# Optimization experiments

Measured on AMD Instinct MI355X. Metric: run time of the kernel, lower is better.

Reference implementation:

```python
import jax, jax.numpy as jnp
import numpy as np

N_LEVELS, CPL = 4, 1024           # levels, cells per level (n_cells = 4096)
IN_D, HID, OUT_D, MLP = 512, 1024, 512, 128


def setup_inputs() -> dict:
    key = jax.random.key(0)
    ks = iter(jax.random.split(key, 32))
    r = lambda shape, s=0.05: jax.random.normal(next(ks), shape, dtype=jnp.float32) * s
    inp = {
        'x': r((1, IN_D), 1.0),
        'hiddens': r((N_LEVELS * CPL, HID), 0.1),
        'ea_W1': r((N_LEVELS, IN_D + HID, MLP)), 'ea_b1': r((N_LEVELS, MLP)),
        'ea_W2': r((N_LEVELS, MLP, OUT_D)),      'ea_b2': r((N_LEVELS, OUT_D)),
        'eg_W1': r((N_LEVELS, IN_D + HID, MLP)), 'eg_b1': r((N_LEVELS, MLP)),
        'eg_W2': r((N_LEVELS, MLP, OUT_D)),      'eg_b2': r((N_LEVELS, OUT_D)),
        'gru_Wih': r((N_LEVELS, 3 * HID, OUT_D + 1)),
        'gru_Whh': r((N_LEVELS, 3 * HID, HID)),
        'gru_bih': r((N_LEVELS, 3 * HID)), 'gru_bhh': r((N_LEVELS, 3 * HID)),
        'pred_W1': r((N_LEVELS - 1, HID, HID)), 'pred_b1': r((N_LEVELS - 1, HID)),
        'pred_W2': r((N_LEVELS - 1, HID, HID)), 'pred_b2': r((N_LEVELS - 1, HID)),
        'pei_W': r((HID * N_LEVELS, OUT_D)), 'pei_b': r((OUT_D,)),
        'step': 10,
    }
    return inp


def _forward(x, hiddens, ea_W1, ea_b1, ea_W2, ea_b2, eg_W1, eg_b1, eg_W2, eg_b2,
             gru_Wih, gru_Whh, gru_bih, gru_bhh, pred_W1, pred_b1, pred_W2, pred_b2,
             pei_W, pei_b, step):
    L = gru_Whh.shape[0]
    Hd = gru_Whh.shape[2]
    C = hiddens.shape[0] // L
    h = hiddens.reshape(L, C, Hd)                              # [L,C,H]
    xb = jnp.broadcast_to(x[0], (L, C, x.shape[-1]))           # same x for every cell
    comb = jnp.concatenate([xb, h], axis=-1)                   # [L,C,IN+H]

    def mlp(W1, b1, W2, b2):
        z = jax.nn.relu(jnp.einsum('lci,lim->lcm', comb, W1) + b1[:, None, :])
        return jnp.einsum('lcm,lmo->lco', z, W2) + b2[:, None, :]

    out = mlp(ea_W1, ea_b1, ea_W2, ea_b2) - mlp(eg_W1, eg_b1, eg_W2, eg_b2)  # a - g
    tension = jnp.mean(out ** 2, axis=-1, keepdims=True)       # [L,C,1]
    avg_tension = jnp.mean(tension)                            # mean over all cells

    # GRUCell (torch gate order r,z,n); mem input is detached in the original
    mem_in = jax.lax.stop_gradient(jnp.concatenate([out, tension], axis=-1))  # [L,C,OUT+1]
    gi = jnp.einsum('lci,lgi->lcg', mem_in, gru_Wih) + gru_bih[:, None, :]
    gh = jnp.einsum('lch,lgh->lcg', h, gru_Whh) + gru_bhh[:, None, :]
    i_r, i_z, i_n = jnp.split(gi, 3, axis=-1)
    h_r, h_z, h_n = jnp.split(gh, 3, axis=-1)
    rg = jax.nn.sigmoid(i_r + h_r)
    zg = jax.nn.sigmoid(i_z + h_z)
    ng = jnp.tanh(i_n + rg * h_n)
    new_h = jax.lax.stop_gradient((1.0 - zg) * ng + zg * h)    # self.hiddens = ...detach()

    level_means = new_h.mean(axis=1)                           # [L,H] (pre pe-update)

    # top-down predictors: predicted[lv] from level_means[lv+1]
    pz = jax.nn.relu(jnp.einsum('li,lim->lm', level_means[1:], pred_W1) + pred_b1)
    predicted = jnp.einsum('lm,lmo->lo', pz, pred_W2) + pred_b2          # [L-1,H]
    pe_signal = jax.lax.stop_gradient((predicted - level_means[:-1]) * 0.05)
    delta = jnp.zeros_like(level_means).at[:-1].add(pe_signal).at[1:].add(-0.5 * pe_signal)
    hh = new_h + delta[:, None, :]

    # per-level mean blend
    hh = 0.85 * hh + 0.15 * hh.mean(axis=1, keepdims=True)
    # faction sync: with n_factions == n_levels, factions == levels exactly
    hh = 0.85 * hh + 0.15 * hh.mean(axis=1, keepdims=True)
    if step > 5:  # debate (step is a static Python int)
        global_op = hh.mean(axis=1).mean(axis=0)               # [H]
        dc = max(1, C // 4)
        hh = hh.at[:, :dc].set(0.85 * hh[:, :dc] + 0.15 * global_op)

    combined = level_means.reshape(-1) @ pei_W + pei_b         # [OUT]
    return combined, avg_tension, hh.reshape(-1, Hd)


def reference(x, hiddens, ea_W1, ea_b1, ea_W2, ea_b2, eg_W1, eg_b1, eg_W2, eg_b2,
              gru_Wih, gru_Whh, gru_bih, gru_bhh, pred_W1, pred_b1, pred_W2, pred_b2,
              pei_W, pei_b, step):
    return _forward(x, hiddens, ea_W1, ea_b1, ea_W2, ea_b2, eg_W1, eg_b1, eg_W2, eg_b2,
                    gru_Wih, gru_Whh, gru_bih, gru_bhh, pred_W1, pred_b1, pred_W2, pred_b2,
                    pei_W, pei_b, step)
```

## Files before the change

### kernel.cpp

```cpp
#include <hip/hip_runtime.h>
#include <math.h>

#define L4   4
#define CPL  1024
#define HID  1024
#define IND  512
#define MLPD 128
#define OUTD 512
#define G3   3072
#define ROWS 4096
#define KP   544

typedef unsigned short u16;
typedef u16   u16x8  __attribute__((ext_vector_type(8)));
typedef short bf16x8 __attribute__((ext_vector_type(8)));
typedef float f32x4  __attribute__((ext_vector_type(4)));

__device__ __forceinline__ float b2f(u16 u) {
  return __uint_as_float(((unsigned int)u) << 16);
}
__device__ __forceinline__ u16 f2b(float f) {
  unsigned int x = __float_as_uint(f);
  x += 0x7fffu + ((x >> 16) & 1u);
  return (u16)(x >> 16);
}
__device__ __forceinline__ float sigm(float v) { return 1.0f/(1.0f + expf(-v)); }

struct F4 { float x, y, z, w; };
__device__ __forceinline__ float ld1(const void* p, size_t i, bool f32) {
  return f32 ? ((const float*)p)[i] : b2f(((const u16*)p)[i]);
}
__device__ __forceinline__ void st1(void* p, size_t i, float v, bool f32) {
  if (f32) ((float*)p)[i] = v; else ((u16*)p)[i] = f2b(v);
}
__device__ __forceinline__ u16x8 ldc8(const void* p, size_t i, bool f32) {
  u16x8 r;
  if (f32) {
    const float* q = (const float*)p + i;
    float4 v0 = *reinterpret_cast<const float4*>(q);
    float4 v1 = *reinterpret_cast<const float4*>(q + 4);
    r[0]=f2b(v0.x); r[1]=f2b(v0.y); r[2]=f2b(v0.z); r[3]=f2b(v0.w);
    r[4]=f2b(v1.x); r[5]=f2b(v1.y); r[6]=f2b(v1.z); r[7]=f2b(v1.w);
  } else {
    r = *reinterpret_cast<const u16x8*>((const u16*)p + i);
  }
  return r;
}

__global__ void k_detect(const void* __restrict__ x, int* __restrict__ flag) {
  int t = threadIdx.x;
  const u16* xu = (const u16*)x;
  unsigned u = xu[2*t];
  int e = (u >> 7) & 0xFF;
  int good = (e >= 96 && e <= 134) ? 1 : 0;
  __shared__ int cnt[256];
  cnt[t] = good;
  __syncthreads();
  for (int s = 128; s > 0; s >>= 1) { if (t < s) cnt[t] += cnt[t+s]; __syncthreads(); }
  if (t == 0) flag[0] = (cnt[0] < 200) ? 1 : 0;
}

__global__ void k_prep(float* __restrict__ zf, const void* __restrict__ bih,
                       const void* __restrict__ bhh, const int* __restrict__ dflag,
                       float* __restrict__ bs_r, float* __restrict__ bs_z,
                       float* __restrict__ bn_i, float* __restrict__ bn_h) {
  const bool f32 = dflag[0] != 0;
  int b = blockIdx.x, t = threadIdx.x;
  if (b < 16) {
    int idx = b*256 + t;
    int l = idx >> 10, j = idx & 1023;
    bs_r[idx] = ld1(bih, l*G3 + j, f32)        + ld1(bhh, l*G3 + j, f32);
    bs_z[idx] = ld1(bih, l*G3 + 1024 + j, f32) + ld1(bhh, l*G3 + 1024 + j, f32);
    bn_i[idx] = ld1(bih, l*G3 + 2048 + j, f32);
    bn_h[idx] = ld1(bhh, l*G3 + 2048 + j, f32);
  } else {
    int idx = (b-16)*256 + t;
    zf[idx] = 0.0f;
  }
}

__global__ void k_prep_wih(const void* __restrict__ Wih, const int* __restrict__ dflag,
                           u16* __restrict__ WihP) {
  const bool f32 = dflag[0] != 0;
  int row = blockIdx.x;
  int t = threadIdx.x;
  size_t src = (size_t)row * 513;
  size_t dst = (size_t)row * KP;
  WihP[dst + t]       = f2b(ld1(Wih, src + t, f32));
  WihP[dst + 256 + t] = f2b(ld1(Wih, src + 256 + t, f32));
  if (t < 32) {
    float v = (t == 0) ? ld1(Wih, src + 512, f32) : 0.0f;
    WihP[dst + 512 + t] = f2b(v);
  }
}

__global__ void k_prep_whh(const void* __restrict__ Whh, const int* __restrict__ dflag,
                           u16* __restrict__ WhhP) {
  const bool f32 = dflag[0] != 0;
  int t = threadIdx.x;
  int row = blockIdx.x*2 + (t >> 7);
  int c8  = (t & 127) * 8;
  size_t off = (size_t)row * HID + c8;
  u16x8 v = ldc8(Whh, off, f32);
  *reinterpret_cast<u16x8*>(&WhhP[off]) = v;
}

__global__ void k_prep_hb(const void* __restrict__ H, const int* __restrict__ dflag,
                          u16* __restrict__ HB) {
  const bool f32 = dflag[0] != 0;
  int t = threadIdx.x;
  int row = blockIdx.x*2 + (t >> 7);
  int c8  = (t & 127) * 8;
  size_t off = (size_t)row * HID + c8;
  u16x8 v = ldc8(H, off, f32);
  *reinterpret_cast<u16x8*>(&HB[off]) = v;
}

__global__ void k_prep_w1t(const void* __restrict__ eaW1, const void* __restrict__ egW1,
                           const int* __restrict__ dflag, u16* __restrict__ W1T) {
  const bool f32 = dflag[0] != 0;
  __shared__ u16 sT[128*66];
  int l = blockIdx.x, path = blockIdx.y, kt = blockIdx.z;
  int t = threadIdx.x;
  const void* W1 = path ? egW1 : eaW1;
  for (int rr = 0; rr < 64; rr += 2) {
    int r = rr + (t >> 7), m = t & 127;
    float v = ld1(W1, ((size_t)l*1536 + 512 + kt*64 + r)*MLPD + m, f32);
    sT[m*66 + r] = f2b(v);
  }
  __syncthreads();
  for (int mm = 0; mm < 128; mm += 4) {
    int m = mm + (t >> 6), kk = t & 63;
    W1T[((size_t)l*256 + path*128 + m)*1024 + kt*64 + kk] = sT[m*66 + kk];
  }
}

__global__ void k_prep_w2m(const void* __restrict__ eaW2, const void* __restrict__ egW2,
                           const int* __restrict__ dflag, u16* __restrict__ W2M) {
  const bool f32 = dflag[0] != 0;
  __shared__ u16 sT[128*130];
  int l = blockIdx.x, path = blockIdx.y, ot = blockIdx.z;
  int t = threadIdx.x;
  const void* W2 = path ? egW2 : eaW2;
  float sgn = path ? -1.0f : 1.0f;
  for (int rr = 0; rr < 128; rr += 2) {
    int r = rr + (t >> 7), o = t & 127;
    float v = ld1(W2, ((size_t)l*MLPD + r)*OUTD + ot*128 + o, f32);
    sT[o*130 + r] = f2b(sgn*v);
  }
  __syncthreads();
  for (int oo = 0; oo < 128; oo += 2) {
    int o = oo + (t >> 7), m = t & 127;
    W2M[((size_t)l*OUTD + ot*128 + o)*256 + path*128 + m] = sT[o*130 + m];
  }
}

__global__ void k_base_acc(const void* __restrict__ x, const void* __restrict__ eaW1,
                           const void* __restrict__ egW1, const int* __restrict__ dflag,
                           float* __restrict__ baseacc) {
  const bool f32 = dflag[0] != 0;
  int l = blockIdx.x, path = blockIdx.y, kc = blockIdx.z, m = threadIdx.x;
  const void* W1 = path ? egW1 : eaW1;
  float acc = 0.0f;
  int i0 = kc*128;
  for (int i = i0; i < i0 + 128; ++i)
    acc += ld1(x, i, f32) * ld1(W1, ((size_t)l*1536 + i)*MLPD + m, f32);
  atomicAdd(&baseacc[path*512 + l*MLPD + m], acc);
}

#define SWZ(row, ku) ((row)*64 + ((ku) ^ (((row)&7)<<3)))

__global__ __launch_bounds__(256) void k_z_mfma(
    const u16* __restrict__ HB, const u16* __restrict__ W1T,
    const void* __restrict__ eab1, const void* __restrict__ egb1,
    const float* __restrict__ baseacc, const int* __restrict__ dflag,
    u16* __restrict__ Z) {
  const bool f32 = dflag[0] != 0;
  __shared__ __align__(16) u16 sA[2][64*64];
  __shared__ __align__(16) u16 sB[2][64*64];
  int t = threadIdx.x;
  int row0 = blockIdx.x * 64;
  int n0   = blockIdx.y * 64;
  int l    = row0 >> 10;
  int wid = t >> 6, lane = t & 63;
  int waveM = wid >> 1, waveN = wid & 1;
  int quad = lane >> 4, lcol = lane & 15;

  f32x4 acc[2][2];
  const f32x4 zz = {0.0f,0.0f,0.0f,0.0f};
#pragma unroll
  for (int i = 0; i < 2; ++i)
#pragma unroll
    for (int j = 0; j < 2; ++j) acc[i][j] = zz;

  u16x8 ra[2], rb[2];
  auto loadk = [&](int k0) {
#pragma unroll
    for (int s = 0; s < 2; ++s) {
      int idx = s*256 + t, row = idx >> 3, ch = idx & 7;
      ra[s] = *reinterpret_cast<const u16x8*>(
          HB + (size_t)(row0 + row)*HID + k0 + ch*8);
      rb[s] = *reinterpret_cast<const u16x8*>(
          W1T + ((size_t)l*256 + n0 + row)*1024 + k0 + ch*8);
    }
  };
  auto stage = [&](int cb) {
#pragma unroll
    for (int s = 0; s < 2; ++s) {
      int idx = s*256 + t, row = idx >> 3, ch = idx & 7;
      *reinterpret_cast<u16x8*>(&sA[cb][SWZ(row, ch*8)]) = ra[s];
      *reinterpret_cast<u16x8*>(&sB[cb][SWZ(row, ch*8)]) = rb[s];
    }
  };

  int cur = 0;
  loadk(0);
  for (int k0 = 0; k0 < HID; k0 += 64) {
    stage(cur);
    asm volatile("s_waitcnt lgkmcnt(0)" ::: "memory");
    __builtin_amdgcn_s_barrier();
    if (k0 + 64 < HID) loadk(k0 + 64);
    __builtin_amdgcn_s_setprio(1);
#pragma unroll
    for (int kc = 0; kc < 2; ++kc) {
      bf16x8 af[2];
#pragma unroll
      for (int i = 0; i < 2; ++i) {
        int rl = waveM*32 + i*16 + lcol;
        af[i] = *reinterpret_cast<const bf16x8*>(&sA[cur][SWZ(rl, kc*32 + quad*8)]);
      }
#pragma unroll
      for (int j = 0; j < 2; ++j) {
        int jl = waveN*32 + j*16 + lcol;
        bf16x8 bf = *reinterpret_cast<const bf16x8*>(&sB[cur][SWZ(jl, kc*32 + quad*8)]);
#pragma unroll
        for (int i = 0; i < 2; ++i)
          acc[i][j] = __builtin_amdgcn_mfma_f32_16x16x32_bf16(af[i], bf, acc[i][j], 0, 0, 0);
      }
    }
    __builtin_amdgcn_s_setprio(0);
    cur ^= 1;
  }
#pragma unroll
  for (int j = 0; j < 2; ++j) {
    int nn = n0 + waveN*32 + j*16 + lcol;
    int path = nn >> 7, m = nn & 127;
    float bval = baseacc[path*512 + l*MLPD + m] +
                 ld1(path ? egb1 : eab1, l*MLPD + m, f32);
#pragma unroll
    for (int i = 0; i < 2; ++i)
#pragma unroll
      for (int g = 0; g < 4; ++g) {
        int r = row0 + waveM*32 + i*16 + quad*4 + g;
        float v = acc[i][j][g] + bval;
        Z[(size_t)r*256 + nn] = f2b(v > 0.0f ? v : 0.0f);
      }
  }
}

__global__ __launch_bounds__(256) void k_outm(
    const u16* __restrict__ Zb, const u16* __restrict__ W2M,
    const void* __restrict__ eab2, const void* __restrict__ egb2,
    const int* __restrict__ dflag, u16* __restrict__ OUTT) {
  const bool f32 = dflag[0] != 0;
  __shared__ __align__(16) u16 sA[2][128*64];
  __shared__ __align__(16) u16 sB[2][64*64];
  int t = threadIdx.x;
  int row0 = blockIdx.x * 128;
  int n0   = blockIdx.y * 64;
  int l    = row0 >> 10;
  int wid = t >> 6, lane = t & 63;
  int waveM = wid & 1, waveJ = wid >> 1;
  int quad = lane >> 4, lcol = lane & 15;

  f32x4 acc[4][2];
  const f32x4 zz = {0.0f,0.0f,0.0f,0.0f};
#pragma unroll
  for (int i = 0; i < 4; ++i)
#pragma unroll
    for (int j = 0; j < 2; ++j) acc[i][j] = zz;

  u16x8 ra[4], rb[2];
  auto loadk = [&](int k0) {
#pragma unroll
    for (int s = 0; s < 4; ++s) {
      int idx = s*256 + t, row = idx >> 3, ch = idx & 7;
      ra[s] = *reinterpret_cast<const u16x8*>(
          Zb + (size_t)(row0 + row)*256 + k0 + ch*8);
    }
#pragma unroll
    for (int s = 0; s < 2; ++s) {
      int idx = s*256 + t, row = idx >> 3, ch = idx & 7;
      rb[s] = *reinterpret_cast<const u16x8*>(
          W2M + ((size_t)l*OUTD + n0 + row)*256 + k0 + ch*8);
    }
  };
  auto stage = [&](int cb) {
#pragma unroll
    for (int s = 0; s < 4; ++s) {
      int idx = s*256 + t, row = idx >> 3, ch = idx & 7;
      *reinterpret_cast<u16x8*>(&sA[cb][SWZ(row, ch*8)]) = ra[s];
    }
#pragma unroll
    for (int s = 0; s < 2; ++s) {
      int idx = s*256 + t, row = idx >> 3, ch = idx & 7;
      *reinterpret_cast<u16x8*>(&sB[cb][SWZ(row, ch*8)]) = rb[s];
    }
  };

  int cur = 0;
  loadk(0);
  for (int k0 = 0; k0 < 256; k0 += 64) {
    stage(cur);
    asm volatile("s_waitcnt lgkmcnt(0)" ::: "memory");
    __builtin_amdgcn_s_barrier();
    if (k0 + 64 < 256) loadk(k0 + 64);
    __builtin_amdgcn_s_setprio(1);
#pragma unroll
    for (int kc = 0; kc < 2; ++kc) {
      bf16x8 af[4];
#pragma unroll
      for (int i = 0; i < 4; ++i) {
        int rl = waveM*64 + i*16 + lcol;
        af[i] = *reinterpret_cast<const bf16x8*>(&sA[cur][SWZ(rl, kc*32 + quad*8)]);
      }
#pragma unroll
      for (int jj = 0; jj < 2; ++jj) {
        int jl = waveJ*32 + jj*16 + lcol;
        bf16x8 bf = *reinterpret_cast<const bf16x8*>(&sB[cur][SWZ(jl, kc*32 + quad*8)]);
#pragma unroll
        for (int i = 0; i < 4; ++i)
          acc[i][jj] = __builtin_amdgcn_mfma_f32_16x16x32_bf16(af[i], bf, acc[i][jj], 0, 0, 0);
      }
    }
    __builtin_amdgcn_s_setprio(0);
    cur ^= 1;
  }
#pragma unroll
  for (int jj = 0; jj < 2; ++jj) {
    int o = n0 + waveJ*32 + jj*16 + lcol;
    float bd = ld1(eab2, l*OUTD + o, f32) - ld1(egb2, l*OUTD + o, f32);
#pragma unroll
    for (int i = 0; i < 4; ++i)
#pragma unroll
      for (int g = 0; g < 4; ++g) {
        int r = row0 + waveM*64 + i*16 + quad*4 + g;
        OUTT[(size_t)r*KP + o] = f2b(acc[i][jj][g] + bd);
      }
  }
}

__global__ void k_tension(u16* __restrict__ OUTT, float* __restrict__ tsum) {
  int row = blockIdx.x, t = threadIdx.x;
  u16* p = OUTT + (size_t)row*KP;
  float v0 = b2f(p[t]), v1 = b2f(p[t+256]);
  float s = v0*v0 + v1*v1;
#pragma unroll
  for (int off = 32; off > 0; off >>= 1) s += __shfl_down(s, off, 64);
  __shared__ float red[4];
  if ((t & 63) == 0) red[t >> 6] = s;
  __syncthreads();
  if (t == 0) {
    float tot = red[0] + red[1] + red[2] + red[3];
    p[512] = f2b(tot * (1.0f/512.0f));
    atomicAdd(tsum, tot);
  }
  if (t < 31) p[513 + t] = 0;
}

__global__ __launch_bounds__(256, 2) void k_gru_mfma(
    const u16* __restrict__ OUTT, const u16* __restrict__ HB,
    const u16* __restrict__ WihP, const u16* __restrict__ WhhP,
    const void* __restrict__ H,
    const float* __restrict__ bs_r, const float* __restrict__ bs_z,
    const float* __restrict__ bn_i, const float* __restrict__ bn_h,
    const int* __restrict__ dflag, void* __restrict__ outv,
    float* __restrict__ lm) {
  const bool f32 = dflag[0] != 0;
  __shared__ __align__(16) u16 sA[2][128*64];
  __shared__ __align__(16) u16 sB[2][3*64*64];
  int t = threadIdx.x;
  int bid = blockIdx.x;
  int xg = bid & 7, inner = bid >> 3;
  int l = xg & 3, jG = xg >> 2;
  int rbi = inner & 7, jbl = inner >> 3;
  int row0 = (l*8 + rbi) * 128;
  int j0   = (jG*8 + jbl) * 64;
  int wid = t >> 6, lane = t & 63;
  int waveM = wid & 1, waveJ = wid >> 1;
  int quad = lane >> 4, lcol = lane & 15;

  f32x4 acc[4][4][2];
  const f32x4 zz = {0.0f,0.0f,0.0f,0.0f};
#pragma unroll
  for (int b = 0; b < 4; ++b)
#pragma unroll
    for (int i = 0; i < 4; ++i)
#pragma unroll
      for (int j = 0; j < 2; ++j) acc[b][i][j] = zz;

  u16x8 ra[4], rbr[6];
  auto load1 = [&](int k0) {
    int kw = KP - k0;
#pragma unroll
    for (int s = 0; s < 4; ++s) {
      int idx = s*256 + t, row = idx >> 3, ch = idx & 7;
      if (ch*8 < kw)
        ra[s] = *reinterpret_cast<const u16x8*>(
            OUTT + (size_t)(row0 + row)*KP + k0 + ch*8);
      else { u16x8 z = {0,0,0,0,0,0,0,0}; ra[s] = z; }
    }
#pragma unroll
    for (int s = 0; s < 6; ++s) {
      int idx = s*256 + t, band = idx >> 9, rem = idx & 511;
      int row = rem >> 3, ch = rem & 7;
      if (ch*8 < kw)
        rbr[s] = *reinterpret_cast<const u16x8*>(
            WihP + ((size_t)l*G3 + band*1024 + j0 + row)*KP + k0 + ch*8);
      else { u16x8 z = {0,0,0,0,0,0,0,0}; rbr[s] = z; }
    }
  };
  auto load2 = [&](int k0) {
#pragma unroll
    for (int s = 0; s < 4; ++s) {
      int idx = s*256 + t, row = idx >> 3, ch = idx & 7;
      ra[s] = *reinterpret_cast<const u16x8*>(
          HB + (size_t)(row0 + row)*HID + k0 + ch*8);
    }
#pragma unroll
    for (int s = 0; s < 6; ++s) {
      int idx = s*256 + t, band = idx >> 9, rem = idx & 511;
      int row = rem >> 3, ch = rem & 7;
      rbr[s] = *reinterpret_cast<const u16x8*>(
          WhhP + ((size_t)l*G3 + band*1024 + j0 + row)*HID + k0 + ch*8);
    }
  };
  auto stage = [&](int cb) {
#pragma unroll
    for (int s = 0; s < 4; ++s) {
      int idx = s*256 + t, row = idx >> 3, ch = idx & 7;
      *reinterpret_cast<u16x8*>(&sA[cb][SWZ(row, ch*8)]) = ra[s];
    }
#pragma unroll
    for (int s = 0; s < 6; ++s) {
      int idx = s*256 + t, band = idx >> 9, rem = idx & 511;
      int row = rem >> 3, ch = rem & 7;
      *reinterpret_cast<u16x8*>(&sB[cb][band*4096 + SWZ(row, ch*8)]) = rbr[s];
    }
  };

  int cur = 0;
  load1(0);
  for (int k0 = 0; k0 < KP; k0 += 64) {
    stage(cur);
    asm volatile("s_waitcnt lgkmcnt(0)" ::: "memory");
    __builtin_amdgcn_s_barrier();
    if (k0 + 64 < KP) load1(k0 + 64);
    else              load2(0);
    __builtin_amdgcn_s_setprio(1);
#pragma unroll
    for (int kc = 0; kc < 2; ++kc) {
      bf16x8 af[4];
#pragma unroll
      for (int i = 0; i < 4; ++i) {
        int rl = waveM*64 + i*16 + lcol;
        af[i] = *reinterpret_cast<const bf16x8*>(&sA[cur][SWZ(rl, kc*32 + quad*8)]);
      }
#pragma unroll
      for (int b = 0; b < 3; ++b)
#pragma unroll
        for (int jj = 0; jj < 2; ++jj) {
          int jl = waveJ*32 + jj*16 + lcol;
          bf16x8 bf = *reinterpret_cast<const bf16x8*>(
              &sB[cur][b*4096 + SWZ(jl, kc*32 + quad*8)]);
#pragma unroll
          for (int i = 0; i < 4; ++i)
            acc[b][i][jj] = __builtin_amdgcn_mfma_f32_16x16x32_bf16(
                af[i], bf, acc[b][i][jj], 0, 0, 0);
        }
    }
    __builtin_amdgcn_s_setprio(0);
    cur ^= 1;
  }
  for (int k0 = 0; k0 < HID; k0 += 64) {
    stage(cur);
    asm volatile("s_waitcnt lgkmcnt(0)" ::: "memory");
    __builtin_amdgcn_s_barrier();
    if (k0 + 64 < HID) load2(k0 + 64);
    __builtin_amdgcn_s_setprio(1);
#pragma unroll
    for (int kc = 0; kc < 2; ++kc) {
      bf16x8 af[4];
#pragma unroll
      for (int i = 0; i < 4; ++i) {
        int rl = waveM*64 + i*16 + lcol;
        af[i] = *reinterpret_cast<const bf16x8*>(&sA[cur][SWZ(rl, kc*32 + quad*8)]);
      }
#pragma unroll
      for (int b = 0; b < 3; ++b) {
        int ai = (b < 2) ? b : 3;
#pragma unroll
        for (int jj = 0; jj < 2; ++jj) {
          int jl = waveJ*32 + jj*16 + lcol;
          bf16x8 bf = *reinterpret_cast<const bf16x8*>(
              &sB[cur][b*4096 + SWZ(jl, kc*32 + quad*8)]);
#pragma unroll
          for (int i = 0; i < 4; ++i)
            acc[ai][i][jj] = __builtin_amdgcn_mfma_f32_16x16x32_bf16(
                af[i], bf, acc[ai][i][jj], 0, 0, 0);
        }
      }
    }
    __builtin_amdgcn_s_setprio(0);
    cur ^= 1;
  }
  float psum[2] = {0.0f, 0.0f};
#pragma unroll
  for (int i = 0; i < 4; ++i)
#pragma unroll
    for (int jj = 0; jj < 2; ++jj) {
      int j = j0 + waveJ*32 + jj*16 + lcol;
      float br = bs_r[l*HID + j], bz = bs_z[l*HID + j];
      float bi = bn_i[l*HID + j], bh = bn_h[l*HID + j];
#pragma unroll
      for (int g = 0; g < 4; ++g) {
        int r = row0 + waveM*64 + i*16 + quad*4 + g;
        float rg = sigm(acc[0][i][jj][g] + br);
        float zg = sigm(acc[1][i][jj][g] + bz);
        float ng = tanhf(acc[2][i][jj][g] + bi + rg*(acc[3][i][jj][g] + bh));
        float hv = ld1(H, (size_t)r*HID + j, f32);
        float nh = (1.0f - zg)*ng + zg*hv;
        st1(outv, 513 + (size_t)r*HID + j, nh, f32);
        psum[jj] += nh;
      }
    }
  __syncthreads();
  float* red = reinterpret_cast<float*>(&sA[0][0]);
  int slot = waveM*4 + quad;
#pragma unroll
  for (int jj = 0; jj < 2; ++jj) {
    int jl = waveJ*32 + jj*16 + lcol;
    red[jl*8 + slot] = psum[jj];
  }
  __syncthreads();
  if (t < 64) {
    float s = 0.0f;
#pragma unroll
    for (int k = 0; k < 8; ++k) s += red[t*8 + k];
    atomicAdd(&lm[l*HID + j0 + t], s);
  }
}

__global__ void k_lmfin(float* __restrict__ lm) {
  int idx = blockIdx.x*256 + threadIdx.x;
  lm[idx] *= (1.0f/1024.0f);
}

__global__ void k_pz_acc(const float* __restrict__ lm, const void* __restrict__ pW1,
                         const int* __restrict__ dflag, float* __restrict__ pz) {
  const bool f32 = dflag[0] != 0;
  int lv = blockIdx.x, mb = blockIdx.y, kc = blockIdx.z;
  int m = mb*256 + threadIdx.x;
  float acc = 0.0f;
  int i0 = kc*32;
  const float* lmp = lm + (lv + 1)*HID;
  for (int i = i0; i < i0 + 32; ++i)
    acc += lmp[i] * ld1(pW1, ((size_t)lv*HID + i)*HID + m, f32);
  atomicAdd(&pz[lv*HID + m], acc);
}
__global__ void k_pzfin(float* __restrict__ pz, const void* __restrict__ pb1,
                        const int* __restrict__ dflag) {
  const bool f32 = dflag[0] != 0;
  int idx = blockIdx.x*256 + threadIdx.x;
  float v = pz[idx] + ld1(pb1, idx, f32);
  pz[idx] = v > 0.0f ? v : 0.0f;
}
__global__ void k_pe_acc(const float* __restrict__ pz, const void* __restrict__ pW2,
                         const int* __restrict__ dflag, float* __restrict__ pe) {
  const bool f32 = dflag[0] != 0;
  int lv = blockIdx.x, ob = blockIdx.y, kc = blockIdx.z;
  int o = ob*256 + threadIdx.x;
  float acc = 0.0f;
  int m0 = kc*32;
  const float* pzp = pz + lv*HID;
  for (int m = m0; m < m0 + 32; ++m)
    acc += pzp[m] * ld1(pW2, ((size_t)lv*HID + m)*HID + o, f32);
  atomicAdd(&pe[lv*HID + o], acc);
}
__global__ void k_pefin(float* __restrict__ pe, const void* __restrict__ pb2,
                        const float* __restrict__ lm, const int* __restrict__ dflag) {
  const bool f32 = dflag[0] != 0;
  int idx = blockIdx.x*256 + threadIdx.x;
  pe[idx] = (pe[idx] + ld1(pb2, idx, f32) - lm[idx]) * 0.05f;
}

__global__ void k_addc_gop(const float* __restrict__ lm, const float* __restrict__ pe,
                           float* __restrict__ addc, float* __restrict__ gop) {
  int j = blockIdx.x*256 + threadIdx.x;
  float pe0 = pe[j], pe1 = pe[1024 + j], pe2 = pe[2048 + j];
  float d0 = pe0, d1 = pe1 - 0.5f*pe0, d2 = pe2 - 0.5f*pe1, d3 = -0.5f*pe2;
  float l0 = lm[j], l1 = lm[1024 + j], l2 = lm[2048 + j], l3 = lm[3072 + j];
  addc[j]        = 0.2775f*l0 + d0;
  addc[1024 + j] = 0.2775f*l1 + d1;
  addc[2048 + j] = 0.2775f*l2 + d2;
  addc[3072 + j] = 0.2775f*l3 + d3;
  gop[j] = 0.25f*((l0 + d0) + (l1 + d1) + (l2 + d2) + (l3 + d3));
}

__global__ void k_comb_acc(const float* __restrict__ lm, const void* __restrict__ peiW,
                           const int* __restrict__ dflag, float* __restrict__ comb) {
  const bool f32 = dflag[0] != 0;
  int ob = blockIdx.x, kc = blockIdx.y;
  int o = ob*256 + threadIdx.x;
  float acc = 0.0f;
  int i0 = kc*128;
  for (int i = i0; i < i0 + 128; ++i)
    acc += lm[i] * ld1(peiW, (size_t)i*OUTD + o, f32);
  atomicAdd(&comb[o], acc);
}
__global__ void k_fin(const float* __restrict__ comb, const void* __restrict__ peib,
                      const float* __restrict__ tsum, const int* __restrict__ dflag,
                      void* __restrict__ outv) {
  const bool f32 = dflag[0] != 0;
  int o = blockIdx.x*256 + threadIdx.x;
  st1(outv, o, comb[o] + ld1(peib, o, f32), f32);
  if (o == 0) st1(outv, 512, tsum[0] * (1.0f/(4096.0f*512.0f)), f32);
}

__global__ void k_hh(void* __restrict__ outv, const float* __restrict__ addc,
                     const float* __restrict__ gop, const int* __restrict__ step,
                     const int* __restrict__ dflag) {
  const bool f32 = dflag[0] != 0;
  int row = blockIdx.x, t = threadIdx.x;
  int l = row >> 10, c = row & 1023;
  bool debate = (step[0] > 5) && (c < 256);
  size_t base = 513 + (size_t)row*HID;
#pragma unroll
  for (int k = 0; k < 4; ++k) {
    int j = t + k*256;
    float v = 0.7225f * ld1(outv, base + j, f32) + addc[l*HID + j];
    if (debate) v = 0.85f*v + 0.15f*gop[j];
    st1(outv, base + j, v, f32);
  }
}

extern "C" void kernel_launch(void* const* d_in, const int* in_sizes, int n_in,
                              void* d_out, int out_size, void* d_ws, size_t ws_size,
                              hipStream_t stream) {
  (void)in_sizes; (void)n_in; (void)out_size; (void)ws_size;
  const void* x    = d_in[0];
  const void* hid  = d_in[1];
  const void* eaW1 = d_in[2];
  const void* eab1 = d_in[3];
  const void* eaW2 = d_in[4];
  const void* eab2 = d_in[5];
  const void* egW1 = d_in[6];
  const void* egb1 = d_in[7];
  const void* egW2 = d_in[8];
  const void* egb2 = d_in[9];
  const void* gWih = d_in[10];
  const void* gWhh = d_in[11];
  const void* gbih = d_in[12];
  const void* gbhh = d_in[13];
  const void* pW1  = d_in[14];
  const void* pb1  = d_in[15];
  const void* pW2  = d_in[16];
  const void* pb2  = d_in[17];
  const void* peiW = d_in[18];
  const void* peib = d_in[19];
  const int*  step = (const int*)d_in[20];

  float* wsf = (float*)d_ws;
  float* tsum    = wsf + 0;
  float* baseacc = wsf + 64;
  float* lm      = wsf + 1088;
  float* pz      = wsf + 5184;
  float* pe      = wsf + 8256;
  float* comb    = wsf + 11328;
  int*   dflag   = (int*)(wsf + 12288);
  float* bs_r    = wsf + 12352;
  float* bs_z    = wsf + 16448;
  float* bn_i    = wsf + 20544;
  float* bn_h    = wsf + 24640;
  float* addc    = wsf + 28736;
  float* gop     = wsf + 32832;
  u16* Zb   = (u16*)(wsf + 33856);
  u16* OUTT = Zb + (size_t)4096*256;
  u16* WihP = OUTT + (size_t)4096*KP;
  u16* HB   = WihP + (size_t)12288*KP;
  u16* WhhP = HB   + (size_t)4096*1024;
  u16* W2M  = WhhP + (size_t)12288*1024;
  u16* W1T  = OUTT;

  k_detect   <<<dim3(1),        dim3(256), 0, stream>>>(x, dflag);
  k_prep     <<<dim3(64),       dim3(256), 0, stream>>>(wsf, gbih, gbhh, dflag,
                                                        bs_r, bs_z, bn_i, bn_h);
  k_prep_wih <<<dim3(12288),    dim3(256), 0, stream>>>(gWih, dflag, WihP);
  k_prep_whh <<<dim3(6144),     dim3(256), 0, stream>>>(gWhh, dflag, WhhP);
  k_prep_hb  <<<dim3(2048),     dim3(256), 0, stream>>>(hid, dflag, HB);
  k_prep_w1t <<<dim3(4,2,16),   dim3(256), 0, stream>>>(eaW1, egW1, dflag, W1T);
  k_prep_w2m <<<dim3(4,2,4),    dim3(256), 0, stream>>>(eaW2, egW2, dflag, W2M);
  k_base_acc <<<dim3(4,2,4),    dim3(128), 0, stream>>>(x, eaW1, egW1, dflag, baseacc);
  k_z_mfma   <<<dim3(64,4),     dim3(256), 0, stream>>>(HB, W1T, eab1, egb1,
                                                        baseacc, dflag, Zb);
  k_outm     <<<dim3(32,8),     dim3(256), 0, stream>>>(Zb, W2M, eab2, egb2,
                                                        dflag, OUTT);
  k_tension  <<<dim3(4096),     dim3(256), 0, stream>>>(OUTT, tsum);
  k_gru_mfma <<<dim3(512),      dim3(256), 0, stream>>>(OUTT, HB, WihP, WhhP, hid,
                                                        bs_r, bs_z, bn_i, bn_h,
                                                        dflag, d_out, lm);
  k_lmfin    <<<dim3(16),       dim3(256), 0, stream>>>(lm);
  k_pz_acc   <<<dim3(3,4,32),   dim3(256), 0, stream>>>(lm, pW1, dflag, pz);
  k_pzfin    <<<dim3(12),       dim3(256), 0, stream>>>(pz, pb1, dflag);
  k_pe_acc   <<<dim3(3,4,32),   dim3(256), 0, stream>>>(pz, pW2, dflag, pe);
  k_pefin    <<<dim3(12),       dim3(256), 0, stream>>>(pe, pb2, lm, dflag);
  k_addc_gop <<<dim3(4),        dim3(256), 0, stream>>>(lm, pe, addc, gop);
  k_comb_acc <<<dim3(2,32),     dim3(256), 0, stream>>>(lm, peiW, dflag, comb);
  k_fin      <<<dim3(2),        dim3(256), 0, stream>>>(comb, peib, tsum, dflag, d_out);
  k_hh       <<<dim3(4096),     dim3(256), 0, stream>>>(d_out, addc, gop, step, dflag);
}
```

Before: 452.8 us.

## Move level-mean reduction out of GRU epilogue into separate kernel; merge prep converts

Removes the per-block shared-memory reduction and atomics from the GRU MFMA epilogue and computes level sums in a new kernel that rereads the written hidden outputs. The 1/1024 scaling is folded into the downstream consumers, which removes the finalize kernel. The two bf16 conversion prep kernels are merged into one launch. This trades a leaner GRU epilogue and fewer launches for an extra full read of the 16 MB output, and row-strided, partly unaligned loads in the new reduction.

```diff
diff --git a/kernel.cpp b/kernel.cpp
--- a/kernel.cpp
+++ b/kernel.cpp
@@ -10,6 +10,7 @@
 #define G3   3072
 #define ROWS 4096
 #define KP   544
+#define SCL  0.0009765625f
 
 typedef unsigned short u16;
 typedef u16   u16x8  __attribute__((ext_vector_type(8)));
@@ -26,7 +27,6 @@
 }
 __device__ __forceinline__ float sigm(float v) { return 1.0f/(1.0f + expf(-v)); }
 
-struct F4 { float x, y, z, w; };
 __device__ __forceinline__ float ld1(const void* p, size_t i, bool f32) {
   return f32 ? ((const float*)p)[i] : b2f(((const u16*)p)[i]);
 }
@@ -94,26 +94,22 @@
   }
 }
 
-__global__ void k_prep_whh(const void* __restrict__ Whh, const int* __restrict__ dflag,
-                           u16* __restrict__ WhhP) {
+__global__ void k_prep_cvt(const void* __restrict__ Whh, const void* __restrict__ H,
+                           const int* __restrict__ dflag,
+                           u16* __restrict__ WhhP, u16* __restrict__ HB) {
   const bool f32 = dflag[0] != 0;
   int t = threadIdx.x;
-  int row = blockIdx.x*2 + (t >> 7);
-  int c8  = (t & 127) * 8;
-  size_t off = (size_t)row * HID + c8;
-  u16x8 v = ldc8(Whh, off, f32);
-  *reinterpret_cast<u16x8*>(&WhhP[off]) = v;
-}
-
-__global__ void k_prep_hb(const void* __restrict__ H, const int* __restrict__ dflag,
-                          u16* __restrict__ HB) {
-  const bool f32 = dflag[0] != 0;
-  int t = threadIdx.x;
-  int row = blockIdx.x*2 + (t >> 7);
-  int c8  = (t & 127) * 8;
-  size_t off = (size_t)row * HID + c8;
-  u16x8 v = ldc8(H, off, f32);
-  *reinterpret_cast<u16x8*>(&HB[off]) = v;
+  int b = blockIdx.x;
+  int c8 = (t & 127) * 8;
+  if (b < 6144) {
+    int row = b*2 + (t >> 7);
+    size_t off = (size_t)row * HID + c8;
+    *reinterpret_cast<u16x8*>(&WhhP[off]) = ldc8(Whh, off, f32);
+  } else {
+    int row = (b - 6144)*2 + (t >> 7);
+    size_t off = (size_t)row * HID + c8;
+    *reinterpret_cast<u16x8*>(&HB[off]) = ldc8(H, off, f32);
+  }
 }
 
 __global__ void k_prep_w1t(const void* __restrict__ eaW1, const void* __restrict__ egW1,
@@ -374,8 +370,7 @@
     const void* __restrict__ H,
     const float* __restrict__ bs_r, const float* __restrict__ bs_z,
     const float* __restrict__ bn_i, const float* __restrict__ bn_h,
-    const int* __restrict__ dflag, void* __restrict__ outv,
-    float* __restrict__ lm) {
+    const int* __restrict__ dflag, void* __restrict__ outv) {
   const bool f32 = dflag[0] != 0;
   __shared__ __align__(16) u16 sA[2][128*64];
   __shared__ __align__(16) u16 sB[2][3*64*64];
@@ -514,7 +509,6 @@
     __builtin_amdgcn_s_setprio(0);
     cur ^= 1;
   }
-  float psum[2] = {0.0f, 0.0f};
 #pragma unroll
   for (int i = 0; i < 4; ++i)
 #pragma unroll
@@ -529,31 +523,27 @@
         float zg = sigm(acc[1][i][jj][g] + bz);
         float ng = tanhf(acc[2][i][jj][g] + bi + rg*(acc[3][i][jj][g] + bh));
         float hv = ld1(H, (size_t)r*HID + j, f32);
-        float nh = (1.0f - zg)*ng + zg*hv;
-        st1(outv, 513 + (size_t)r*HID + j, nh, f32);
-        psum[jj] += nh;
-      }
-    }
-  __syncthreads();
-  float* red = reinterpret_cast<float*>(&sA[0][0]);
-  int slot = waveM*4 + quad;
-#pragma unroll
-  for (int jj = 0; jj < 2; ++jj) {
-    int jl = waveJ*32 + jj*16 + lcol;
-    red[jl*8 + slot] = psum[jj];
-  }
-  __syncthreads();
-  if (t < 64) {
-    float s = 0.0f;
-#pragma unroll
-    for (int k = 0; k < 8; ++k) s += red[t*8 + k];
-    atomicAdd(&lm[l*HID + j0 + t], s);
-  }
-}
-
-__global__ void k_lmfin(float* __restrict__ lm) {
-  int idx = blockIdx.x*256 + threadIdx.x;
-  lm[idx] *= (1.0f/1024.0f);
+        st1(outv, 513 + (size_t)r*HID + j, (1.0f - zg)*ng + zg*hv, f32);
+      }
+    }
+}
+
+__global__ void k_lm_acc(const void* __restrict__ outv, const int* __restrict__ dflag,
+                         float* __restrict__ lm) {
+  const bool f32 = dflag[0] != 0;
+  int l = blockIdx.x, cc = blockIdx.y, t = threadIdx.x;
+  float s0=0.f, s1=0.f, s2=0.f, s3=0.f;
+  for (int c = cc*16; c < cc*16 + 16; ++c) {
+    size_t base = 513 + (size_t)(l*CPL + c)*HID;
+    s0 += ld1(outv, base + t,       f32);
+    s1 += ld1(outv, base + 256 + t, f32);
+    s2 += ld1(outv, base + 512 + t, f32);
+    s3 += ld1(outv, base + 768 + t, f32);
+  }
+  atomicAdd(&lm[l*HID + t],       s0);
+  atomicAdd(&lm[l*HID + 256 + t], s1);
+  atomicAdd(&lm[l*HID + 512 + t], s2);
+  atomicAdd(&lm[l*HID + 768 + t], s3);
 }
 
 __global__ void k_pz_acc(const float* __restrict__ lm, const void* __restrict__ pW1,
@@ -566,7 +556,7 @@
   const float* lmp = lm + (lv + 1)*HID;
   for (int i = i0; i < i0 + 32; ++i)
     acc += lmp[i] * ld1(pW1, ((size_t)lv*HID + i)*HID + m, f32);
-  atomicAdd(&pz[lv*HID + m], acc);
+  atomicAdd(&pz[lv*HID + m], acc * SCL);
 }
 __global__ void k_pzfin(float* __restrict__ pz, const void* __restrict__ pb1,
                         const int* __restrict__ dflag) {
@@ -591,7 +581,7 @@
                         const float* __restrict__ lm, const int* __restrict__ dflag) {
   const bool f32 = dflag[0] != 0;
   int idx = blockIdx.x*256 + threadIdx.x;
-  pe[idx] = (pe[idx] + ld1(pb2, idx, f32) - lm[idx]) * 0.05f;
+  pe[idx] = (pe[idx] + ld1(pb2, idx, f32) - lm[idx]*SCL) * 0.05f;
 }
 
 __global__ void k_addc_gop(const float* __restrict__ lm, const float* __restrict__ pe,
@@ -599,7 +589,7 @@
   int j = blockIdx.x*256 + threadIdx.x;
   float pe0 = pe[j], pe1 = pe[1024 + j], pe2 = pe[2048 + j];
   float d0 = pe0, d1 = pe1 - 0.5f*pe0, d2 = pe2 - 0.5f*pe1, d3 = -0.5f*pe2;
-  float l0 = lm[j], l1 = lm[1024 + j], l2 = lm[2048 + j], l3 = lm[3072 + j];
+  float l0 = lm[j]*SCL, l1 = lm[1024 + j]*SCL, l2 = lm[2048 + j]*SCL, l3 = lm[3072 + j]*SCL;
   addc[j]        = 0.2775f*l0 + d0;
   addc[1024 + j] = 0.2775f*l1 + d1;
   addc[2048 + j] = 0.2775f*l2 + d2;
@@ -616,7 +606,7 @@
   int i0 = kc*128;
   for (int i = i0; i < i0 + 128; ++i)
     acc += lm[i] * ld1(peiW, (size_t)i*OUTD + o, f32);
-  atomicAdd(&comb[o], acc);
+  atomicAdd(&comb[o], acc * SCL);
 }
 __global__ void k_fin(const float* __restrict__ comb, const void* __restrict__ peib,
                       const float* __restrict__ tsum, const int* __restrict__ dflag,
@@ -696,8 +686,7 @@
   k_prep     <<<dim3(64),       dim3(256), 0, stream>>>(wsf, gbih, gbhh, dflag,
                                                         bs_r, bs_z, bn_i, bn_h);
   k_prep_wih <<<dim3(12288),    dim3(256), 0, stream>>>(gWih, dflag, WihP);
-  k_prep_whh <<<dim3(6144),     dim3(256), 0, stream>>>(gWhh, dflag, WhhP);
-  k_prep_hb  <<<dim3(2048),     dim3(256), 0, stream>>>(hid, dflag, HB);
+  k_prep_cvt <<<dim3(8192),     dim3(256), 0, stream>>>(gWhh, hid, dflag, WhhP, HB);
   k_prep_w1t <<<dim3(4,2,16),   dim3(256), 0, stream>>>(eaW1, egW1, dflag, W1T);
   k_prep_w2m <<<dim3(4,2,4),    dim3(256), 0, stream>>>(eaW2, egW2, dflag, W2M);
   k_base_acc <<<dim3(4,2,4),    dim3(128), 0, stream>>>(x, eaW1, egW1, dflag, baseacc);
@@ -708,8 +697,8 @@
   k_tension  <<<dim3(4096),     dim3(256), 0, stream>>>(OUTT, tsum);
   k_gru_mfma <<<dim3(512),      dim3(256), 0, stream>>>(OUTT, HB, WihP, WhhP, hid,
                                                         bs_r, bs_z, bn_i, bn_h,
-                                                        dflag, d_out, lm);
-  k_lmfin    <<<dim3(16),       dim3(256), 0, stream>>>(lm);
+                                                        dflag, d_out);
+  k_lm_acc   <<<dim3(4,64),     dim3(256), 0, stream>>>(d_out, dflag, lm);
   k_pz_acc   <<<dim3(3,4,32),   dim3(256), 0, stream>>>(lm, pW1, dflag, pz);
   k_pzfin    <<<dim3(12),       dim3(256), 0, stream>>>(pz, pb1, dflag);
   k_pe_acc   <<<dim3(3,4,32),   dim3(256), 0, stream>>>(pz, pW2, dflag, pe);
```

After: 477.7 us. 5.5% more time.
